# Kernel tuning notes

Hardware: AMD Instinct MI355X
Metric: run time of the kernel (lower is better)

## Reference

```python
import jax, jax.numpy as jnp
import numpy as np


def _row_distance(a, b):
    # pairwise cosine similarity between rows of a [N,D] and b [K,D] -> [N,K]
    an = a / (jnp.linalg.norm(a, axis=1, keepdims=True) + 1e-12)
    bn = b / (jnp.linalg.norm(b, axis=1, keepdims=True) + 1e-12)
    return an @ bn.T


def _nearest_context(feature, context):
    sim = _row_distance(feature, context)          # [B, K]
    # distances = -sim; argmin(distances) == argmax(sim)
    min_ind = jnp.argmax(sim, axis=1)              # [B]
    onehot = jax.nn.one_hot(min_ind, context.shape[0], dtype=feature.dtype)  # [B, K]
    rslt = onehot @ jax.lax.stop_gradient(context)  # [B, E] codebook gather
    return rslt, onehot


@jax.custom_vjp
def _vq(feature, context):
    return _nearest_context(feature, context)[0]


def _vq_fwd(feature, context):
    value, ind = _nearest_context(feature, context)
    return value, ind


def _vq_bwd(ind, d_value):
    # straight-through to feature; scatter grads into codebook rows
    return (d_value, ind.T @ d_value)


_vq.defvjp(_vq_fwd, _vq_bwd)


def setup_inputs() -> dict:
    key = jax.random.key(0)
    ks = jax.random.split(key, 6)
    B, FEAT, MID, EMB, K = 8192, 4096, 512, 256, 512
    return {
        "x": jax.random.normal(ks[0], (B, FEAT), dtype=jnp.float32),
        "enc_w1": jax.random.normal(ks[1], (FEAT, MID), dtype=jnp.float32) * 0.02,
        "enc_b1": jnp.zeros((MID,), dtype=jnp.float32),
        "enc_w2": jax.random.normal(ks[2], (MID, EMB), dtype=jnp.float32) * 0.02,
        "enc_b2": jnp.zeros((EMB,), dtype=jnp.float32),
        "emb": jax.random.normal(ks[3], (K, EMB), dtype=jnp.float32) * 0.01,
        "dec_w1": jax.random.normal(ks[4], (EMB, MID), dtype=jnp.float32) * 0.02,
        "dec_b1": jnp.zeros((MID,), dtype=jnp.float32),
        "dec_w2": jax.random.normal(ks[5], (MID, FEAT), dtype=jnp.float32) * 0.02,
        "dec_b2": jnp.zeros((FEAT,), dtype=jnp.float32),
    }


def reference(x, enc_w1, enc_b1, enc_w2, enc_b2, emb, dec_w1, dec_b1, dec_w2, dec_b2):
    # encoder (stand-in for MultiContextEncoder with out_size=(middle_dim, emb_dim))
    h = jax.nn.relu(x @ enc_w1 + enc_b1)           # [B, MID]
    encoded = h @ enc_w2 + enc_b2                  # [B, EMB]
    # vector quantization with straight-through gradient
    vq_feat = _vq(encoded, emb)                    # [B, EMB]
    _, context_ind = _nearest_context(encoded, emb)  # [B, K] one-hot
    # decoder: Dense(middle_dim, relu) -> Dense(feat_dim, relu)
    d = jax.nn.relu(vq_feat @ dec_w1 + dec_b1)     # [B, MID]
    decoded = jax.nn.relu(d @ dec_w2 + dec_b2)     # [B, FEAT]
    return (encoded, vq_feat, context_ind, decoded, emb)
```

## Files before the change

kernel.cpp:

```cpp
#include <hip/hip_runtime.h>

#define BATCH 8192
#define FEAT  4096
#define MID   512
#define EMB   256
#define KCODE 512

typedef _Float16 half8 __attribute__((ext_vector_type(8)));
typedef _Float16 half4v __attribute__((ext_vector_type(4)));
typedef float floatx4 __attribute__((ext_vector_type(4)));

#define SC_X    512.0f
#define SC_W    4096.0f
#define SC_H    512.0f
#define SC_ENC  4096.0f
#define SC_CODE 4096.0f
#define SC_EMB  4096.0f
#define SC_TM   512.0f
#define DS_G1   (1.0f / (SC_X   * SC_W))
#define DS_G2   (1.0f / (SC_H   * SC_W))
#define DS_D1   (1.0f / (SC_EMB * SC_W))
#define DS_D2   (1.0f / (SC_TM  * SC_W))

#define GLD16(gp, lp)                                                          \
    __builtin_amdgcn_global_load_lds(                                          \
        (const __attribute__((address_space(1))) void*)(gp),                   \
        (__attribute__((address_space(3))) void*)(lp), 16, 0, 0)

template<int NT, int AF32>
__global__ __launch_bounds__(256)
void gemm_sk(const float* __restrict__ Af32,
             const _Float16* __restrict__ Ahg, const _Float16* __restrict__ Alg,
             const _Float16* __restrict__ BTh, const _Float16* __restrict__ BTl,
             float aScale,
             float* __restrict__ partOut,
             const float* __restrict__ bias, float descale, int relu,
             float* __restrict__ outF, _Float16* __restrict__ outHi,
             _Float16* __restrict__ outLo, float outScale,
             int M, int N, int K, int lgK, int lgN, int swz)
{
    __shared__ _Float16 AhS[128 * 32];
    __shared__ _Float16 BhS[128 * 32];
    __shared__ _Float16 AlS[NT == 3 ? 128 * 32 : 8];
    __shared__ _Float16 BlS[NT == 3 ? 128 * 32 : 8];

    const int tid  = threadIdx.x;
    const int lane = tid & 63;
    const int wave = tid >> 6;
    const int wm = wave >> 1, wn = wave & 1;
    const int l15  = lane & 15;
    const int quad = lane >> 4;
    const int q8   = quad * 8;

    int bm, bn, ks;
    if (swz) {
        int b = blockIdx.x;
        int mlo = b & 7;
        ks = (b >> 3) & ((1 << lgK) - 1);
        bn = (b >> (3 + lgK)) & ((1 << lgN) - 1);
        bm = ((b >> (3 + lgK + lgN)) << 3) | mlo;
    } else { bm = blockIdx.y; bn = blockIdx.x; ks = 0; }
    const int row0 = bm * 128, col0 = bn * 128;
    const int Kslice = K >> lgK;
    const int k0 = ks * Kslice;

    const int sr4 = tid >> 2;
    const int sc4 = (tid & 3) * 8;
    const size_t aB0 = (size_t)(row0 + sr4) * K + sc4;
    const size_t aB1 = (size_t)(row0 + 64 + sr4) * K + sc4;
    const size_t bB0 = (size_t)(col0 + sr4) * K + sc4;
    const size_t bB1 = (size_t)(col0 + 64 + sr4) * K + sc4;
    const int l0 = tid * 8, l1 = 2048 + tid * 8;

    const int sr2 = tid >> 1;
    const int sk2 = (tid & 1) * 16;
    const size_t aOff2 = (size_t)(row0 + sr2) * K + sk2;
    const int lA = sr2 * 32 + sk2;

    floatx4 acc[4][4] = {};

    for (int kt = 0; kt < Kslice; kt += 32) {
        GLD16(BTh + bB0 + k0 + kt, &BhS[l0]);
        GLD16(BTh + bB1 + k0 + kt, &BhS[l1]);
        if (NT == 3) {
            GLD16(BTl + bB0 + k0 + kt, &BlS[l0]);
            GLD16(BTl + bB1 + k0 + kt, &BlS[l1]);
        }
        if (AF32) {
            const float* p = Af32 + aOff2 + k0 + kt;
            float4 f0 = *(const float4*)(p);
            float4 f1 = *(const float4*)(p + 4);
            float4 f2 = *(const float4*)(p + 8);
            float4 f3 = *(const float4*)(p + 12);
            float fv[16] = {f0.x,f0.y,f0.z,f0.w, f1.x,f1.y,f1.z,f1.w,
                            f2.x,f2.y,f2.z,f2.w, f3.x,f3.y,f3.z,f3.w};
            half8 hv0, hv1, lv0, lv1;
            #pragma unroll
            for (int e = 0; e < 8; ++e) {
                float v = fv[e] * aScale;
                _Float16 h = (_Float16)v;
                hv0[e] = h; lv0[e] = (_Float16)(v - (float)h);
            }
            #pragma unroll
            for (int e = 0; e < 8; ++e) {
                float v = fv[8 + e] * aScale;
                _Float16 h = (_Float16)v;
                hv1[e] = h; lv1[e] = (_Float16)(v - (float)h);
            }
            *(half8*)&AhS[lA] = hv0; *(half8*)&AhS[lA + 8] = hv1;
            if (NT == 3) { *(half8*)&AlS[lA] = lv0; *(half8*)&AlS[lA + 8] = lv1; }
        } else {
            GLD16(Ahg + aB0 + k0 + kt, &AhS[l0]);
            GLD16(Ahg + aB1 + k0 + kt, &AhS[l1]);
            if (NT == 3) {
                GLD16(Alg + aB0 + k0 + kt, &AlS[l0]);
                GLD16(Alg + aB1 + k0 + kt, &AlS[l1]);
            }
        }
        __syncthreads();

        half8 ah[4], al4[4], bh[4], bl4[4];
        #pragma unroll
        for (int i = 0; i < 4; ++i) {
            int ra = (wm * 64 + i * 16 + l15) * 32 + q8;
            int rb = (wn * 64 + i * 16 + l15) * 32 + q8;
            ah[i] = *(const half8*)&AhS[ra];
            bh[i] = *(const half8*)&BhS[rb];
            if (NT == 3) {
                al4[i] = *(const half8*)&AlS[ra];
                bl4[i] = *(const half8*)&BlS[rb];
            }
        }
        #pragma unroll
        for (int i = 0; i < 4; ++i)
            #pragma unroll
            for (int j = 0; j < 4; ++j) {
                acc[i][j] = __builtin_amdgcn_mfma_f32_16x16x32_f16(ah[i], bh[j], acc[i][j], 0, 0, 0);
                if (NT == 3) {
                    acc[i][j] = __builtin_amdgcn_mfma_f32_16x16x32_f16(ah[i],  bl4[j], acc[i][j], 0, 0, 0);
                    acc[i][j] = __builtin_amdgcn_mfma_f32_16x16x32_f16(al4[i], bh[j],  acc[i][j], 0, 0, 0);
                }
            }
        __syncthreads();
    }

    if (partOut) {
        float* po = partOut + (size_t)ks * M * N;
        #pragma unroll
        for (int j = 0; j < 4; ++j) {
            int col = col0 + wn * 64 + j * 16 + l15;
            #pragma unroll
            for (int i = 0; i < 4; ++i)
                #pragma unroll
                for (int t = 0; t < 4; ++t) {
                    int r = row0 + wm * 64 + i * 16 + quad * 4 + t;
                    po[(size_t)r * N + col] = acc[i][j][t];
                }
        }
    } else {
        #pragma unroll
        for (int j = 0; j < 4; ++j) {
            int col = col0 + wn * 64 + j * 16 + l15;
            float bcol = bias ? bias[col] : 0.0f;
            #pragma unroll
            for (int i = 0; i < 4; ++i)
                #pragma unroll
                for (int t = 0; t < 4; ++t) {
                    int r = row0 + wm * 64 + i * 16 + quad * 4 + t;
                    float v = acc[i][j][t] * descale + bcol;
                    if (relu) v = fmaxf(v, 0.0f);
                    size_t o = (size_t)r * N + col;
                    if (outF) outF[o] = v;
                    if (outHi) {
                        float sv = v * outScale;
                        _Float16 h = (_Float16)sv;
                        outHi[o] = h;
                        outLo[o] = (_Float16)(sv - (float)h);
                    }
                }
        }
    }
}

__global__ __launch_bounds__(256)
void reduce_sk(const float* __restrict__ part, int nSlice, int MN, int N,
               const float* __restrict__ bias, float descale, int relu,
               float* __restrict__ outF, _Float16* __restrict__ outHi,
               _Float16* __restrict__ outLo, float outScale)
{
    int i = blockIdx.x * 256 + threadIdx.x;
    if (i * 4 >= MN) return;
    float4 s = ((const float4*)part)[i];
    for (int sl = 1; sl < nSlice; ++sl) {
        float4 p = ((const float4*)(part + (size_t)sl * MN))[i];
        s.x += p.x; s.y += p.y; s.z += p.z; s.w += p.w;
    }
    int col = (i * 4) % N;
    float v[4] = {s.x, s.y, s.z, s.w};
    #pragma unroll
    for (int e = 0; e < 4; ++e) {
        float t = v[e] * descale + (bias ? bias[col + e] : 0.0f);
        if (relu) t = fmaxf(t, 0.0f);
        v[e] = t;
    }
    if (outF) ((float4*)outF)[i] = *(float4*)v;
    if (outHi) {
        half4v hv, lv;
        #pragma unroll
        for (int e = 0; e < 4; ++e) {
            float sv = v[e] * outScale;
            _Float16 h = (_Float16)sv;
            hv[e] = h;
            lv[e] = (_Float16)(sv - (float)h);
        }
        ((half4v*)outHi)[i] = hv;
        ((half4v*)outLo)[i] = lv;
    }
}

__global__ __launch_bounds__(256)
void transpose_split(const float* __restrict__ src, _Float16* __restrict__ hi,
                     _Float16* __restrict__ lo, float scale, int R, int C)
{
    __shared__ float t[32][33];
    int tx = threadIdx.x & 31, ty = threadIdx.x >> 5;
    int r0 = blockIdx.y * 32, c0 = blockIdx.x * 32;
    #pragma unroll
    for (int p = 0; p < 4; ++p) {
        int r = ty + p * 8;
        t[r][tx] = src[(size_t)(r0 + r) * C + c0 + tx];
    }
    __syncthreads();
    #pragma unroll
    for (int p = 0; p < 4; ++p) {
        int oc = ty + p * 8;
        float v = t[tx][oc] * scale;
        _Float16 h = (_Float16)v;
        size_t o = (size_t)(c0 + oc) * R + r0 + tx;
        hi[o] = h;
        lo[o] = (_Float16)(v - (float)h);
    }
}

__global__ __launch_bounds__(256)
void norm_codes(const float* __restrict__ emb, _Float16* __restrict__ cnHi,
                _Float16* __restrict__ cnLo)
{
    int wave = threadIdx.x >> 6;
    int lane = threadIdx.x & 63;
    int c = blockIdx.x * 4 + wave;
    if (c >= KCODE) return;
    const float* er = emb + (size_t)c * EMB;
    float ss = 0.0f;
    #pragma unroll
    for (int k = lane; k < EMB; k += 64) { float v = er[k]; ss += v * v; }
    #pragma unroll
    for (int off = 32; off > 0; off >>= 1) ss += __shfl_down(ss, off, 64);
    ss = __shfl(ss, 0, 64);
    float inv = 1.0f / (sqrtf(ss) + 1e-12f);
    #pragma unroll
    for (int k = lane; k < EMB; k += 64) {
        float v = er[k] * inv * SC_CODE;
        _Float16 h = (_Float16)v;
        cnHi[(size_t)c * EMB + k] = h;
        cnLo[(size_t)c * EMB + k] = (_Float16)(v - (float)h);
    }
}

__global__ __launch_bounds__(256)
void argmax_vq2(const float* __restrict__ part, int MN,
                const float* __restrict__ emb,
                float* __restrict__ onehot, float* __restrict__ vqfeat,
                int* __restrict__ idxOut)
{
    int wave = threadIdx.x >> 6;
    int lane = threadIdx.x & 63;
    int row = blockIdx.x * 4 + wave;
    if (row >= BATCH) return;

    const float* p0 = part + (size_t)row * KCODE;
    const float* p1 = part + (size_t)MN + (size_t)row * KCODE;
    float bestV = -3.402823466e+38f;
    int   bestI = 0;
    #pragma unroll
    for (int c = lane; c < KCODE; c += 64) {
        float v = p0[c] + p1[c];
        if (v > bestV) { bestV = v; bestI = c; }
    }
    #pragma unroll
    for (int off = 32; off > 0; off >>= 1) {
        float ov = __shfl_down(bestV, off, 64);
        int   oi = __shfl_down(bestI, off, 64);
        if (ov > bestV || (ov == bestV && oi < bestI)) { bestV = ov; bestI = oi; }
    }
    bestI = __shfl(bestI, 0, 64);
    if (lane == 0) idxOut[row] = bestI;

    float* oh = onehot + (size_t)row * KCODE;
    #pragma unroll
    for (int c = lane; c < KCODE; c += 64) oh[c] = (c == bestI) ? 1.0f : 0.0f;

    const float* er = emb + (size_t)bestI * EMB;
    float* vr = vqfeat + (size_t)row * EMB;
    #pragma unroll
    for (int c = lane; c < EMB; c += 64) vr[c] = er[c];
}

__global__ __launch_bounds__(256)
void gather_decoded(const float* __restrict__ Dcode, const int* __restrict__ idx,
                    float* __restrict__ out)
{
    int row = blockIdx.x;
    int k = idx[row];
    const float4* src = (const float4*)(Dcode + (size_t)k * FEAT);
    float4* dst = (float4*)(out + (size_t)row * FEAT);
    #pragma unroll
    for (int i = threadIdx.x; i < FEAT / 4; i += 256) dst[i] = src[i];
}

__global__ __launch_bounds__(256)
void copy_f4(const float* __restrict__ src, float* __restrict__ dst, int n4)
{
    int i = blockIdx.x * 256 + threadIdx.x;
    if (i < n4) ((float4*)dst)[i] = ((const float4*)src)[i];
}

extern "C" void kernel_launch(void* const* d_in, const int* in_sizes, int n_in,
                              void* d_out, int out_size, void* d_ws, size_t ws_size,
                              hipStream_t stream)
{
    const float* x      = (const float*)d_in[0];
    const float* enc_w1 = (const float*)d_in[1];
    const float* enc_b1 = (const float*)d_in[2];
    const float* enc_w2 = (const float*)d_in[3];
    const float* enc_b2 = (const float*)d_in[4];
    const float* emb    = (const float*)d_in[5];
    const float* dec_w1 = (const float*)d_in[6];
    const float* dec_b1 = (const float*)d_in[7];
    const float* dec_w2 = (const float*)d_in[8];
    const float* dec_b2 = (const float*)d_in[9];

    float* out = (float*)d_out;
    float* out_encoded = out;
    float* out_vqfeat  = out + (size_t)BATCH * EMB;
    float* out_onehot  = out + (size_t)2 * BATCH * EMB;
    float* out_decoded = out + (size_t)2 * BATCH * EMB + (size_t)BATCH * KCODE;
    float* out_emb     = out_decoded + (size_t)BATCH * FEAT;

    char* w = (char*)d_ws;
    _Float16* w1T_hi = (_Float16*)w;  w += (size_t)FEAT * MID * 2;
    _Float16* w1T_lo = (_Float16*)w;  w += (size_t)FEAT * MID * 2;
    _Float16* w2T_hi = (_Float16*)w;  w += (size_t)MID * EMB * 2;
    _Float16* w2T_lo = (_Float16*)w;  w += (size_t)MID * EMB * 2;
    _Float16* wd1T_hi= (_Float16*)w;  w += (size_t)MID * EMB * 2;
    _Float16* wd1T_lo= (_Float16*)w;  w += (size_t)MID * EMB * 2;
    _Float16* wd2T_hi= (_Float16*)w;  w += (size_t)FEAT * MID * 2;
    _Float16* wd2T_lo= (_Float16*)w;  w += (size_t)FEAT * MID * 2;
    _Float16* h_hi   = (_Float16*)w;  w += (size_t)BATCH * MID * 2;
    _Float16* h_lo   = (_Float16*)w;  w += (size_t)BATCH * MID * 2;
    _Float16* enc_hi = (_Float16*)w;  w += (size_t)BATCH * EMB * 2;
    _Float16* enc_lo = (_Float16*)w;  w += (size_t)BATCH * EMB * 2;
    _Float16* cn_hi  = (_Float16*)w;  w += (size_t)KCODE * EMB * 2;
    _Float16* cn_lo  = (_Float16*)w;  w += (size_t)KCODE * EMB * 2;
    _Float16* tm_hi  = (_Float16*)w;  w += (size_t)KCODE * MID * 2;
    _Float16* tm_lo  = (_Float16*)w;  w += (size_t)KCODE * MID * 2;
    float*    Dc     = (float*)w;     w += (size_t)KCODE * FEAT * 4;
    float*    scr    = (float*)w;     w += (size_t)4 * BATCH * MID * 4;
    int*      idx    = (int*)w;

    transpose_split<<<dim3(MID / 32, FEAT / 32), dim3(256), 0, stream>>>(
        enc_w1, w1T_hi, w1T_lo, SC_W, FEAT, MID);
    transpose_split<<<dim3(EMB / 32, MID / 32), dim3(256), 0, stream>>>(
        enc_w2, w2T_hi, w2T_lo, SC_W, MID, EMB);
    transpose_split<<<dim3(MID / 32, EMB / 32), dim3(256), 0, stream>>>(
        dec_w1, wd1T_hi, wd1T_lo, SC_W, EMB, MID);
    transpose_split<<<dim3(FEAT / 32, MID / 32), dim3(256), 0, stream>>>(
        dec_w2, wd2T_hi, wd2T_lo, SC_W, MID, FEAT);
    norm_codes<<<dim3(KCODE / 4), dim3(256), 0, stream>>>(emb, cn_hi, cn_lo);
    copy_f4<<<dim3((KCODE * EMB / 4 + 255) / 256), dim3(256), 0, stream>>>(
        emb, out_emb, KCODE * EMB / 4);

    gemm_sk<3, 1><<<dim3(1024), dim3(256), 0, stream>>>(
        x, nullptr, nullptr, w1T_hi, w1T_lo, SC_X,
        scr, nullptr, 0.0f, 0, nullptr, nullptr, nullptr, 0.0f,
        BATCH, MID, FEAT, 2, 2, 1);
    reduce_sk<<<dim3(BATCH * MID / 4 / 256), dim3(256), 0, stream>>>(
        scr, 4, BATCH * MID, MID, enc_b1, DS_G1, 1,
        nullptr, h_hi, h_lo, SC_H);

    gemm_sk<3, 0><<<dim3(512), dim3(256), 0, stream>>>(
        nullptr, h_hi, h_lo, w2T_hi, w2T_lo, 0.0f,
        scr, nullptr, 0.0f, 0, nullptr, nullptr, nullptr, 0.0f,
        BATCH, EMB, MID, 2, 1, 1);
    reduce_sk<<<dim3(BATCH * EMB / 4 / 256), dim3(256), 0, stream>>>(
        scr, 4, BATCH * EMB, EMB, enc_b2, DS_G2, 0,
        out_encoded, enc_hi, enc_lo, SC_ENC);

    gemm_sk<3, 0><<<dim3(512), dim3(256), 0, stream>>>(
        nullptr, enc_hi, enc_lo, cn_hi, cn_lo, 0.0f,
        scr, nullptr, 0.0f, 0, nullptr, nullptr, nullptr, 0.0f,
        BATCH, KCODE, EMB, 1, 2, 1);
    argmax_vq2<<<dim3(BATCH / 4), dim3(256), 0, stream>>>(
        scr, BATCH * KCODE, emb, out_onehot, out_vqfeat, idx);

    gemm_sk<1, 1><<<dim3(KCODE / 128, KCODE / 128), dim3(256), 0, stream>>>(
        emb, nullptr, nullptr, wd1T_hi, wd1T_lo, SC_EMB,
        nullptr, dec_b1, DS_D1, 1, nullptr, tm_hi, tm_lo, SC_TM,
        KCODE, MID, EMB, 0, 0, 0);
    gemm_sk<1, 0><<<dim3(FEAT / 128, KCODE / 128), dim3(256), 0, stream>>>(
        nullptr, tm_hi, tm_lo, wd2T_hi, wd2T_lo, 0.0f,
        nullptr, dec_b2, DS_D2, 1, Dc, nullptr, nullptr, 0.0f,
        KCODE, FEAT, MID, 0, 0, 0);

    gather_decoded<<<dim3(BATCH), dim3(256), 0, stream>>>(Dc, idx, out_decoded);
}
```

Before: 498.7 us.

## Fold codebook similarity into encoder GEMM and register-prefetch A tiles

```diff
diff --git a/kernel.cpp b/kernel.cpp
--- a/kernel.cpp
+++ b/kernel.cpp
@@ -5,6 +5,7 @@
 #define MID   512
 #define EMB   256
 #define KCODE 512
+#define N23   768
 
 typedef _Float16 half8 __attribute__((ext_vector_type(8)));
 typedef _Float16 half4v __attribute__((ext_vector_type(4)));
@@ -13,14 +14,16 @@
 #define SC_X    512.0f
 #define SC_W    4096.0f
 #define SC_H    512.0f
-#define SC_ENC  4096.0f
 #define SC_CODE 4096.0f
+#define SC_T    4096.0f
 #define SC_EMB  4096.0f
 #define SC_TM   512.0f
-#define DS_G1   (1.0f / (SC_X   * SC_W))
-#define DS_G2   (1.0f / (SC_H   * SC_W))
-#define DS_D1   (1.0f / (SC_EMB * SC_W))
-#define DS_D2   (1.0f / (SC_TM  * SC_W))
+#define DS_G1   (1.0f / (SC_X    * SC_W))
+#define DS_ENC  (1.0f / (SC_H    * SC_W))
+#define DS_S    (1.0f / (SC_H    * SC_T))
+#define DS_T    (1.0f / (SC_CODE * SC_W))
+#define DS_D1   (1.0f / (SC_EMB  * SC_W))
+#define DS_D2   (1.0f / (SC_TM   * SC_W))
 
 #define GLD16(gp, lp)                                                          \
     __builtin_amdgcn_global_load_lds(                                          \
@@ -59,15 +62,13 @@
         ks = (b >> 3) & ((1 << lgK) - 1);
         bn = (b >> (3 + lgK)) & ((1 << lgN) - 1);
         bm = ((b >> (3 + lgK + lgN)) << 3) | mlo;
-    } else { bm = blockIdx.y; bn = blockIdx.x; ks = 0; }
+    } else { bn = blockIdx.x; bm = blockIdx.y; ks = blockIdx.z; }
     const int row0 = bm * 128, col0 = bn * 128;
     const int Kslice = K >> lgK;
     const int k0 = ks * Kslice;
 
     const int sr4 = tid >> 2;
     const int sc4 = (tid & 3) * 8;
-    const size_t aB0 = (size_t)(row0 + sr4) * K + sc4;
-    const size_t aB1 = (size_t)(row0 + 64 + sr4) * K + sc4;
     const size_t bB0 = (size_t)(col0 + sr4) * K + sc4;
     const size_t bB1 = (size_t)(col0 + 64 + sr4) * K + sc4;
     const int l0 = tid * 8, l1 = 2048 + tid * 8;
@@ -78,47 +79,62 @@
     const int lA = sr2 * 32 + sk2;
 
     floatx4 acc[4][4] = {};
-
-    for (int kt = 0; kt < Kslice; kt += 32) {
-        GLD16(BTh + bB0 + k0 + kt, &BhS[l0]);
-        GLD16(BTh + bB1 + k0 + kt, &BhS[l1]);
-        if (NT == 3) {
-            GLD16(BTl + bB0 + k0 + kt, &BlS[l0]);
-            GLD16(BTl + bB1 + k0 + kt, &BlS[l1]);
-        }
+    float4 fa[2][4];
+    half8  rah[2][2], ral[2][2];
+
+    auto loadA = [&](int s, int kt) {
         if (AF32) {
             const float* p = Af32 + aOff2 + k0 + kt;
-            float4 f0 = *(const float4*)(p);
-            float4 f1 = *(const float4*)(p + 4);
-            float4 f2 = *(const float4*)(p + 8);
-            float4 f3 = *(const float4*)(p + 12);
-            float fv[16] = {f0.x,f0.y,f0.z,f0.w, f1.x,f1.y,f1.z,f1.w,
-                            f2.x,f2.y,f2.z,f2.w, f3.x,f3.y,f3.z,f3.w};
+            fa[s][0] = *(const float4*)(p);
+            fa[s][1] = *(const float4*)(p + 4);
+            fa[s][2] = *(const float4*)(p + 8);
+            fa[s][3] = *(const float4*)(p + 12);
+        } else {
+            const _Float16* p = Ahg + aOff2 + k0 + kt;
+            rah[s][0] = *(const half8*)(p);
+            rah[s][1] = *(const half8*)(p + 8);
+            if (NT == 3) {
+                const _Float16* q = Alg + aOff2 + k0 + kt;
+                ral[s][0] = *(const half8*)(q);
+                ral[s][1] = *(const half8*)(q + 8);
+            }
+        }
+    };
+
+    auto writeA = [&](int s) {
+        if (AF32) {
+            const float* f = (const float*)&fa[s][0];
             half8 hv0, hv1, lv0, lv1;
             #pragma unroll
             for (int e = 0; e < 8; ++e) {
-                float v = fv[e] * aScale;
+                float v = f[e] * aScale;
                 _Float16 h = (_Float16)v;
                 hv0[e] = h; lv0[e] = (_Float16)(v - (float)h);
             }
             #pragma unroll
             for (int e = 0; e < 8; ++e) {
-                float v = fv[8 + e] * aScale;
+                float v = f[8 + e] * aScale;
                 _Float16 h = (_Float16)v;
                 hv1[e] = h; lv1[e] = (_Float16)(v - (float)h);
             }
             *(half8*)&AhS[lA] = hv0; *(half8*)&AhS[lA + 8] = hv1;
             if (NT == 3) { *(half8*)&AlS[lA] = lv0; *(half8*)&AlS[lA + 8] = lv1; }
         } else {
-            GLD16(Ahg + aB0 + k0 + kt, &AhS[l0]);
-            GLD16(Ahg + aB1 + k0 + kt, &AhS[l1]);
-            if (NT == 3) {
-                GLD16(Alg + aB0 + k0 + kt, &AlS[l0]);
-                GLD16(Alg + aB1 + k0 + kt, &AlS[l1]);
-            }
-        }
-        __syncthreads();
-
+            *(half8*)&AhS[lA] = rah[s][0]; *(half8*)&AhS[lA + 8] = rah[s][1];
+            if (NT == 3) { *(half8*)&AlS[lA] = ral[s][0]; *(half8*)&AlS[lA + 8] = ral[s][1]; }
+        }
+    };
+
+    auto stageB = [&](int kt) {
+        GLD16(BTh + bB0 + k0 + kt, &BhS[l0]);
+        GLD16(BTh + bB1 + k0 + kt, &BhS[l1]);
+        if (NT == 3) {
+            GLD16(BTl + bB0 + k0 + kt, &BlS[l0]);
+            GLD16(BTl + bB1 + k0 + kt, &BlS[l1]);
+        }
+    };
+
+    auto computeTile = [&]() {
         half8 ah[4], al4[4], bh[4], bl4[4];
         #pragma unroll
         for (int i = 0; i < 4; ++i) {
@@ -141,6 +157,22 @@
                     acc[i][j] = __builtin_amdgcn_mfma_f32_16x16x32_f16(al4[i], bh[j],  acc[i][j], 0, 0, 0);
                 }
             }
+    };
+
+    const int nIter = Kslice / 32;
+    loadA(0, 0);
+    for (int it = 0; it < nIter; it += 2) {
+        writeA(0);
+        stageB(it * 32);
+        __syncthreads();
+        if (it + 1 < nIter) loadA(1, (it + 1) * 32);
+        computeTile();
+        __syncthreads();
+        writeA(1);
+        stageB((it + 1) * 32);
+        __syncthreads();
+        if (it + 2 < nIter) loadA(0, (it + 2) * 32);
+        computeTile();
         __syncthreads();
     }
 
@@ -185,8 +217,8 @@
 __global__ __launch_bounds__(256)
 void reduce_sk(const float* __restrict__ part, int nSlice, int MN, int N,
                const float* __restrict__ bias, float descale, int relu,
-               float* __restrict__ outF, _Float16* __restrict__ outHi,
-               _Float16* __restrict__ outLo, float outScale)
+               _Float16* __restrict__ outHi, _Float16* __restrict__ outLo,
+               float outScale)
 {
     int i = blockIdx.x * 256 + threadIdx.x;
     if (i * 4 >= MN) return;
@@ -197,25 +229,18 @@
     }
     int col = (i * 4) % N;
     float v[4] = {s.x, s.y, s.z, s.w};
+    half4v hv, lv;
     #pragma unroll
     for (int e = 0; e < 4; ++e) {
         float t = v[e] * descale + (bias ? bias[col + e] : 0.0f);
         if (relu) t = fmaxf(t, 0.0f);
-        v[e] = t;
-    }
-    if (outF) ((float4*)outF)[i] = *(float4*)v;
-    if (outHi) {
-        half4v hv, lv;
-        #pragma unroll
-        for (int e = 0; e < 4; ++e) {
-            float sv = v[e] * outScale;
-            _Float16 h = (_Float16)sv;
-            hv[e] = h;
-            lv[e] = (_Float16)(sv - (float)h);
-        }
-        ((half4v*)outHi)[i] = hv;
-        ((half4v*)outLo)[i] = lv;
-    }
+        float sv = t * outScale;
+        _Float16 h = (_Float16)sv;
+        hv[e] = h;
+        lv[e] = (_Float16)(sv - (float)h);
+    }
+    ((half4v*)outHi)[i] = hv;
+    ((half4v*)outLo)[i] = lv;
 }
 
 __global__ __launch_bounds__(256)
@@ -243,21 +268,53 @@
 }
 
 __global__ __launch_bounds__(256)
-void norm_codes(const float* __restrict__ emb, _Float16* __restrict__ cnHi,
-                _Float16* __restrict__ cnLo)
+void split_plain(const float* __restrict__ src, _Float16* __restrict__ hi,
+                 _Float16* __restrict__ lo, float scale, int n8)
+{
+    int i = blockIdx.x * 256 + threadIdx.x;
+    if (i >= n8) return;
+    const float4* s4 = (const float4*)src;
+    float4 a = s4[i * 2], b = s4[i * 2 + 1];
+    float v[8] = {a.x, a.y, a.z, a.w, b.x, b.y, b.z, b.w};
+    half8 hv, lv;
+    #pragma unroll
+    for (int j = 0; j < 8; ++j) {
+        float sv = v[j] * scale;
+        _Float16 h = (_Float16)sv;
+        hv[j] = h;
+        lv[j] = (_Float16)(sv - (float)h);
+    }
+    ((half8*)hi)[i] = hv;
+    ((half8*)lo)[i] = lv;
+}
+
+__global__ __launch_bounds__(256)
+void norm_codes(const float* __restrict__ emb, const float* __restrict__ b2,
+                _Float16* __restrict__ cnHi, _Float16* __restrict__ cnLo,
+                float* __restrict__ outEmb, float* __restrict__ bias3)
 {
     int wave = threadIdx.x >> 6;
     int lane = threadIdx.x & 63;
     int c = blockIdx.x * 4 + wave;
     if (c >= KCODE) return;
     const float* er = emb + (size_t)c * EMB;
-    float ss = 0.0f;
-    #pragma unroll
-    for (int k = lane; k < EMB; k += 64) { float v = er[k]; ss += v * v; }
-    #pragma unroll
-    for (int off = 32; off > 0; off >>= 1) ss += __shfl_down(ss, off, 64);
+    float ss = 0.0f, sb = 0.0f;
+    #pragma unroll
+    for (int k = lane; k < EMB; k += 64) {
+        float v = er[k];
+        ss += v * v;
+        sb += v * b2[k];
+        outEmb[(size_t)c * EMB + k] = v;
+    }
+    #pragma unroll
+    for (int off = 32; off > 0; off >>= 1) {
+        ss += __shfl_down(ss, off, 64);
+        sb += __shfl_down(sb, off, 64);
+    }
     ss = __shfl(ss, 0, 64);
+    sb = __shfl(sb, 0, 64);
     float inv = 1.0f / (sqrtf(ss) + 1e-12f);
+    if (lane == 0) bias3[c] = sb * inv;
     #pragma unroll
     for (int k = lane; k < EMB; k += 64) {
         float v = er[k] * inv * SC_CODE;
@@ -268,23 +325,28 @@
 }
 
 __global__ __launch_bounds__(256)
-void argmax_vq2(const float* __restrict__ part, int MN,
-                const float* __restrict__ emb,
-                float* __restrict__ onehot, float* __restrict__ vqfeat,
-                int* __restrict__ idxOut)
+void finish_vq(const float* __restrict__ part, const float* __restrict__ b2,
+               const float* __restrict__ bias3, const float* __restrict__ emb,
+               float* __restrict__ outEnc, float* __restrict__ onehot,
+               float* __restrict__ vqfeat, int* __restrict__ idxOut)
 {
     int wave = threadIdx.x >> 6;
     int lane = threadIdx.x & 63;
     int row = blockIdx.x * 4 + wave;
     if (row >= BATCH) return;
 
-    const float* p0 = part + (size_t)row * KCODE;
-    const float* p1 = part + (size_t)MN + (size_t)row * KCODE;
+    const float* p0 = part + (size_t)row * N23;
+    const float* p1 = part + (size_t)BATCH * N23 + (size_t)row * N23;
+
+    #pragma unroll
+    for (int c = lane; c < EMB; c += 64)
+        outEnc[(size_t)row * EMB + c] = (p0[c] + p1[c]) * DS_ENC + b2[c];
+
     float bestV = -3.402823466e+38f;
     int   bestI = 0;
     #pragma unroll
     for (int c = lane; c < KCODE; c += 64) {
-        float v = p0[c] + p1[c];
+        float v = (p0[EMB + c] + p1[EMB + c]) * DS_S + bias3[c];
         if (v > bestV) { bestV = v; bestI = c; }
     }
     #pragma unroll
@@ -316,13 +378,6 @@
     float4* dst = (float4*)(out + (size_t)row * FEAT);
     #pragma unroll
     for (int i = threadIdx.x; i < FEAT / 4; i += 256) dst[i] = src[i];
-}
-
-__global__ __launch_bounds__(256)
-void copy_f4(const float* __restrict__ src, float* __restrict__ dst, int n4)
-{
-    int i = blockIdx.x * 256 + threadIdx.x;
-    if (i < n4) ((float4*)dst)[i] = ((const float4*)src)[i];
 }
 
 extern "C" void kernel_launch(void* const* d_in, const int* in_sizes, int n_in,
@@ -350,20 +405,21 @@
     char* w = (char*)d_ws;
     _Float16* w1T_hi = (_Float16*)w;  w += (size_t)FEAT * MID * 2;
     _Float16* w1T_lo = (_Float16*)w;  w += (size_t)FEAT * MID * 2;
-    _Float16* w2T_hi = (_Float16*)w;  w += (size_t)MID * EMB * 2;
-    _Float16* w2T_lo = (_Float16*)w;  w += (size_t)MID * EMB * 2;
+    _Float16* wd2T_hi= (_Float16*)w;  w += (size_t)FEAT * MID * 2;
+    _Float16* wd2T_lo= (_Float16*)w;  w += (size_t)FEAT * MID * 2;
+    _Float16* w2s_hi = (_Float16*)w;  w += (size_t)MID * EMB * 2;
+    _Float16* w2s_lo = (_Float16*)w;  w += (size_t)MID * EMB * 2;
     _Float16* wd1T_hi= (_Float16*)w;  w += (size_t)MID * EMB * 2;
     _Float16* wd1T_lo= (_Float16*)w;  w += (size_t)MID * EMB * 2;
-    _Float16* wd2T_hi= (_Float16*)w;  w += (size_t)FEAT * MID * 2;
-    _Float16* wd2T_lo= (_Float16*)w;  w += (size_t)FEAT * MID * 2;
     _Float16* h_hi   = (_Float16*)w;  w += (size_t)BATCH * MID * 2;
     _Float16* h_lo   = (_Float16*)w;  w += (size_t)BATCH * MID * 2;
-    _Float16* enc_hi = (_Float16*)w;  w += (size_t)BATCH * EMB * 2;
-    _Float16* enc_lo = (_Float16*)w;  w += (size_t)BATCH * EMB * 2;
     _Float16* cn_hi  = (_Float16*)w;  w += (size_t)KCODE * EMB * 2;
     _Float16* cn_lo  = (_Float16*)w;  w += (size_t)KCODE * EMB * 2;
+    _Float16* B23_hi = (_Float16*)w;  w += (size_t)N23 * MID * 2;
+    _Float16* B23_lo = (_Float16*)w;  w += (size_t)N23 * MID * 2;
     _Float16* tm_hi  = (_Float16*)w;  w += (size_t)KCODE * MID * 2;
     _Float16* tm_lo  = (_Float16*)w;  w += (size_t)KCODE * MID * 2;
+    float*    bias3  = (float*)w;     w += (size_t)KCODE * 4;
     float*    Dc     = (float*)w;     w += (size_t)KCODE * FEAT * 4;
     float*    scr    = (float*)w;     w += (size_t)4 * BATCH * MID * 4;
     int*      idx    = (int*)w;
@@ -371,43 +427,42 @@
     transpose_split<<<dim3(MID / 32, FEAT / 32), dim3(256), 0, stream>>>(
         enc_w1, w1T_hi, w1T_lo, SC_W, FEAT, MID);
     transpose_split<<<dim3(EMB / 32, MID / 32), dim3(256), 0, stream>>>(
-        enc_w2, w2T_hi, w2T_lo, SC_W, MID, EMB);
+        enc_w2, B23_hi, B23_lo, SC_W, MID, EMB);
     transpose_split<<<dim3(MID / 32, EMB / 32), dim3(256), 0, stream>>>(
         dec_w1, wd1T_hi, wd1T_lo, SC_W, EMB, MID);
     transpose_split<<<dim3(FEAT / 32, MID / 32), dim3(256), 0, stream>>>(
         dec_w2, wd2T_hi, wd2T_lo, SC_W, MID, FEAT);
-    norm_codes<<<dim3(KCODE / 4), dim3(256), 0, stream>>>(emb, cn_hi, cn_lo);
-    copy_f4<<<dim3((KCODE * EMB / 4 + 255) / 256), dim3(256), 0, stream>>>(
-        emb, out_emb, KCODE * EMB / 4);
+    split_plain<<<dim3(MID * EMB / 8 / 256), dim3(256), 0, stream>>>(
+        enc_w2, w2s_hi, w2s_lo, SC_W, MID * EMB / 8);
+    norm_codes<<<dim3(KCODE / 4), dim3(256), 0, stream>>>(
+        emb, enc_b2, cn_hi, cn_lo, out_emb, bias3);
+
+    gemm_sk<3, 0><<<dim3(MID / 128, KCODE / 128, 1), dim3(256), 0, stream>>>(
+        nullptr, cn_hi, cn_lo, w2s_hi, w2s_lo, 0.0f,
+        nullptr, nullptr, DS_T, 0,
+        nullptr, B23_hi + (size_t)EMB * MID, B23_lo + (size_t)EMB * MID, SC_T,
+        KCODE, MID, EMB, 0, 0, 0);
 
     gemm_sk<3, 1><<<dim3(1024), dim3(256), 0, stream>>>(
         x, nullptr, nullptr, w1T_hi, w1T_lo, SC_X,
         scr, nullptr, 0.0f, 0, nullptr, nullptr, nullptr, 0.0f,
         BATCH, MID, FEAT, 2, 2, 1);
     reduce_sk<<<dim3(BATCH * MID / 4 / 256), dim3(256), 0, stream>>>(
-        scr, 4, BATCH * MID, MID, enc_b1, DS_G1, 1,
-        nullptr, h_hi, h_lo, SC_H);
-
-    gemm_sk<3, 0><<<dim3(512), dim3(256), 0, stream>>>(
-        nullptr, h_hi, h_lo, w2T_hi, w2T_lo, 0.0f,
+        scr, 4, BATCH * MID, MID, enc_b1, DS_G1, 1, h_hi, h_lo, SC_H);
+
+    gemm_sk<3, 0><<<dim3(N23 / 128, BATCH / 128, 2), dim3(256), 0, stream>>>(
+        nullptr, h_hi, h_lo, B23_hi, B23_lo, 0.0f,
         scr, nullptr, 0.0f, 0, nullptr, nullptr, nullptr, 0.0f,
-        BATCH, EMB, MID, 2, 1, 1);
-    reduce_sk<<<dim3(BATCH * EMB / 4 / 256), dim3(256), 0, stream>>>(
-        scr, 4, BATCH * EMB, EMB, enc_b2, DS_G2, 0,
-        out_encoded, enc_hi, enc_lo, SC_ENC);
-
-    gemm_sk<3, 0><<<dim3(512), dim3(256), 0, stream>>>(
-        nullptr, enc_hi, enc_lo, cn_hi, cn_lo, 0.0f,
-        scr, nullptr, 0.0f, 0, nullptr, nullptr, nullptr, 0.0f,
-        BATCH, KCODE, EMB, 1, 2, 1);
-    argmax_vq2<<<dim3(BATCH / 4), dim3(256), 0, stream>>>(
-        scr, BATCH * KCODE, emb, out_onehot, out_vqfeat, idx);
-
-    gemm_sk<1, 1><<<dim3(KCODE / 128, KCODE / 128), dim3(256), 0, stream>>>(
+        BATCH, N23, MID, 1, 0, 0);
+
+    finish_vq<<<dim3(BATCH / 4), dim3(256), 0, stream>>>(
+        scr, enc_b2, bias3, emb, out_encoded, out_onehot, out_vqfeat, idx);
+
+    gemm_sk<1, 1><<<dim3(MID / 128, KCODE / 128, 1), dim3(256), 0, stream>>>(
         emb, nullptr, nullptr, wd1T_hi, wd1T_lo, SC_EMB,
         nullptr, dec_b1, DS_D1, 1, nullptr, tm_hi, tm_lo, SC_TM,
         KCODE, MID, EMB, 0, 0, 0);
-    gemm_sk<1, 0><<<dim3(FEAT / 128, KCODE / 128), dim3(256), 0, stream>>>(
+    gemm_sk<1, 0><<<dim3(FEAT / 128, KCODE / 128, 1), dim3(256), 0, stream>>>(
         nullptr, tm_hi, tm_lo, wd2T_hi, wd2T_lo, 0.0f,
         nullptr, dec_b2, DS_D2, 1, Dc, nullptr, nullptr, 0.0f,
         KCODE, FEAT, MID, 0, 0, 0);
```

Measured after the change: 507.2 us. Within noise of the previous version (+1.7%).
